# Kernel tuning notes

Hardware: AMD Instinct MI355X
Metric: run time of the kernel (lower is better)

Reference implementation:

```python
import jax, jax.numpy as jnp
import numpy as np

# Scalar-only irreps: 8x0e nodes in, 4x0e edge in, 8x0e edge out, 16x0e node out.
N = 50000          # nodes
E = 800000         # edges
MUL_NODE_IN = 8
MUL_EDGE_IN = 4
MUL_Z = 2 * MUL_NODE_IN          # cat([x[i], x[j]]) -> 16
MUL_EDGE_OUT = 8
MUL_NODE_OUT = 16
W_NUMEL = MUL_EDGE_IN * MUL_Z * MUL_EDGE_OUT  # 512 = edge_tp.weight_numel
RAD_IN, RAD_HID = 16, 64         # radial_neurons=[16, 64]


def setup_inputs() -> dict:
    key = jax.random.key(0)
    ks = jax.random.split(key, 7)
    x = jax.random.normal(ks[0], (N, MUL_NODE_IN), dtype=jnp.float32)
    edge_index = jax.random.randint(ks[1], (2, E), 0, N)
    edge_attr = jax.random.normal(ks[2], (E, MUL_EDGE_IN), dtype=jnp.float32)
    edge_len_emb = jax.random.normal(ks[3], (E, RAD_IN), dtype=jnp.float32)
    # radial MLP (e3nn FullyConnectedNet: normalized linear layers, silu)
    w1 = jax.random.normal(ks[4], (RAD_IN, RAD_HID), dtype=jnp.float32)
    w2 = jax.random.normal(ks[5], (RAD_HID, W_NUMEL), dtype=jnp.float32)
    # node_tp internal shared weights: [mul_node_in, mul_edge_out, mul_node_out]
    w_node = jax.random.normal(ks[6], (MUL_NODE_IN, MUL_EDGE_OUT, MUL_NODE_OUT), dtype=jnp.float32)
    return {"x": x, "edge_index": edge_index, "edge_attr": edge_attr,
            "edge_len_emb": edge_len_emb, "w1": w1, "w2": w2, "w_node": w_node}


def reference(x, edge_index, edge_attr, edge_len_emb, w1, w2, w_node):
    i, j = edge_index[0], edge_index[1]
    # radial MLP -> per-edge TP weights (e3nn normalized linears, silu)
    h = jax.nn.silu(edge_len_emb @ w1 / jnp.sqrt(jnp.float32(RAD_IN)))
    w_edge = (h @ w2 / jnp.sqrt(jnp.float32(RAD_HID)))
    w_edge = w_edge.reshape(E, MUL_EDGE_IN, MUL_Z, MUL_EDGE_OUT)
    # gather + concat: z = cat([x[i], x[j]])  [E, 16]
    z = jnp.concatenate([x[i], x[j]], axis=-1)
    # edge_tp: fully-connected scalar TP with path norm 1/sqrt(mul1*mul2)
    edge_out = jnp.einsum('ea,eb,eabk->ek', edge_attr, z, w_edge)
    edge_out = edge_out / jnp.sqrt(jnp.float32(MUL_EDGE_IN * MUL_Z))
    # scatter-sum to destination nodes j
    e_sum = jax.ops.segment_sum(edge_out, j, num_segments=x.shape[0])
    # node_tp: shared internal weights, path norm 1/sqrt(mul1*mul2)
    x_out = jnp.einsum('na,nb,abk->nk', x, e_sum, w_node)
    x_out = x_out / jnp.sqrt(jnp.float32(MUL_NODE_IN * MUL_EDGE_OUT))
    return (x_out, edge_out)
```

## Files before the change

kernel.cpp:

```cpp
#include <hip/hip_runtime.h>


typedef __attribute__((ext_vector_type(8))) short short8;
typedef __attribute__((ext_vector_type(4))) float floatx4;

__device__ inline unsigned short f2bf(float f) {
    union { float f; unsigned u; } v; v.f = f;
    unsigned r = v.u + 0x7FFFu + ((v.u >> 16) & 1u);
    return (unsigned short)(r >> 16);
}
__device__ inline float bf2f(unsigned short u) {
    union { unsigned u; float f; } v; v.u = ((unsigned)u) << 16;
    return v.f;
}

constexpr int TB   = 512;
constexpr int NBLK = 256;

constexpr int W2_LD = 72;
constexpr int HS_LD = 72;
constexpr int ZT_LD = 40;
constexpr int AT_LD = 40;

__global__ __launch_bounds__(TB, 2) void edge_kernel(
    const float* __restrict__ x,
    const int*   __restrict__ ei,
    const float* __restrict__ attr,
    const float* __restrict__ emb,
    const float* __restrict__ w1,
    const float* __restrict__ w2,
    float* __restrict__ edge_out,
    float* __restrict__ e_sum,
    int E)
{
    __shared__ __align__(16) unsigned short s_w2t[512 * W2_LD];
    __shared__ __align__(16) unsigned short s_hsA[8 * 32 * HS_LD];
    __shared__ __align__(16) unsigned short s_ztA[8 * 16 * ZT_LD];
    __shared__ __align__(16) unsigned short s_atA[8 * 4 * AT_LD];
    __shared__ __align__(16) int            s_vjA[8 * 32];

    const int tid  = threadIdx.x;
    const int wave = tid >> 6;
    const int lane = tid & 63;
    const int m16  = lane & 15;
    const int quad = lane >> 4;

    for (int idx = tid; idx < 512 * 64; idx += TB) {
        const int n = idx & 511, k = idx >> 9;
        s_w2t[n * W2_LD + k] = f2bf(w2[k * 512 + n]);
    }
    __syncthreads();

    short8 w1f[4];
    #pragma unroll
    for (int ct = 0; ct < 4; ++ct) {
        short8 f;
        if (quad < 2) {
            #pragma unroll
            for (int j = 0; j < 8; ++j)
                f[j] = (short)f2bf(w1[(quad * 8 + j) * 64 + ct * 16 + m16]);
        } else {
            #pragma unroll
            for (int j = 0; j < 8; ++j) f[j] = 0;
        }
        w1f[ct] = f;
    }

    unsigned short* hsw = s_hsA + wave * 32 * HS_LD;
    unsigned short* ztw = s_ztA + wave * 16 * ZT_LD;
    unsigned short* atw = s_atA + wave * 4 * AT_LD;
    int*            vjw = s_vjA + wave * 32;

    const int wid = blockIdx.x * 8 + wave;
    const int nw  = NBLK * 8;
    const int ntiles = E >> 5;

    for (int tile = wid; tile < ntiles; tile += nw) {
        const int base = tile << 5;

        if (quad < 2) {
            const int mst = quad * 16 + m16;
            const int e   = base + mst;
            const int vj  = ei[E + e];
            const float4 a4  = *(const float4*)(attr + (size_t)e * 4);
            const int vi  = ei[e];
            const float4 xi0 = *(const float4*)(x + (size_t)vi * 8);
            const float4 xi1 = *(const float4*)(x + (size_t)vi * 8 + 4);
            const float4 xj0 = *(const float4*)(x + (size_t)vj * 8);
            const float4 xj1 = *(const float4*)(x + (size_t)vj * 8 + 4);
            ztw[ 0*ZT_LD+mst]=f2bf(xi0.x); ztw[ 1*ZT_LD+mst]=f2bf(xi0.y);
            ztw[ 2*ZT_LD+mst]=f2bf(xi0.z); ztw[ 3*ZT_LD+mst]=f2bf(xi0.w);
            ztw[ 4*ZT_LD+mst]=f2bf(xi1.x); ztw[ 5*ZT_LD+mst]=f2bf(xi1.y);
            ztw[ 6*ZT_LD+mst]=f2bf(xi1.z); ztw[ 7*ZT_LD+mst]=f2bf(xi1.w);
            ztw[ 8*ZT_LD+mst]=f2bf(xj0.x); ztw[ 9*ZT_LD+mst]=f2bf(xj0.y);
            ztw[10*ZT_LD+mst]=f2bf(xj0.z); ztw[11*ZT_LD+mst]=f2bf(xj0.w);
            ztw[12*ZT_LD+mst]=f2bf(xj1.x); ztw[13*ZT_LD+mst]=f2bf(xj1.y);
            ztw[14*ZT_LD+mst]=f2bf(xj1.z); ztw[15*ZT_LD+mst]=f2bf(xj1.w);
            atw[0*AT_LD+mst]=f2bf(a4.x);   atw[1*AT_LD+mst]=f2bf(a4.y);
            atw[2*AT_LD+mst]=f2bf(a4.z);   atw[3*AT_LD+mst]=f2bf(a4.w);
            vjw[mst] = vj;
        }

        short8 a1[2];
        #pragma unroll
        for (int s = 0; s < 2; ++s) {
            short8 f;
            if (quad < 2) {
                const float* ep = emb + (size_t)(base + s * 16 + m16) * 16 + quad * 8;
                const float4 u0 = *(const float4*)ep;
                const float4 u1 = *(const float4*)(ep + 4);
                f[0]=(short)f2bf(u0.x); f[1]=(short)f2bf(u0.y);
                f[2]=(short)f2bf(u0.z); f[3]=(short)f2bf(u0.w);
                f[4]=(short)f2bf(u1.x); f[5]=(short)f2bf(u1.y);
                f[6]=(short)f2bf(u1.z); f[7]=(short)f2bf(u1.w);
            } else {
                #pragma unroll
                for (int j = 0; j < 8; ++j) f[j] = 0;
            }
            a1[s] = f;
        }

        #pragma unroll
        for (int s = 0; s < 2; ++s) {
            #pragma unroll
            for (int ct = 0; ct < 4; ++ct) {
                floatx4 c = {0.f, 0.f, 0.f, 0.f};
                c = __builtin_amdgcn_mfma_f32_16x16x32_bf16(a1[s], w1f[ct], c, 0, 0, 0);
                #pragma unroll
                for (int r = 0; r < 4; ++r) {
                    const float u  = c[r] * 0.25f;
                    const float sv = u / (1.f + __expf(-u)) * (1.0f / 64.0f);
                    hsw[(s * 16 + quad * 4 + r) * HS_LD + ct * 16 + m16] = f2bf(sv);
                }
            }
        }

        short8 a2[2][2];
        #pragma unroll
        for (int s = 0; s < 2; ++s)
            #pragma unroll
            for (int q = 0; q < 2; ++q)
                a2[s][q] = *(const short8*)(hsw + (s * 16 + m16) * HS_LD + q * 32 + quad * 8);

        float eacc[2][4];
        #pragma unroll
        for (int s = 0; s < 2; ++s)
            #pragma unroll
            for (int r = 0; r < 4; ++r) eacc[s][r] = 0.f;

        #pragma unroll 1
        for (int g = 0; g < 4; ++g) {
            float av[2][4];
            #pragma unroll
            for (int s = 0; s < 2; ++s) {
                const ushort4 a4v = *(const ushort4*)(atw + g * AT_LD + s * 16 + quad * 4);
                av[s][0] = bf2f(a4v.x); av[s][1] = bf2f(a4v.y);
                av[s][2] = bf2f(a4v.z); av[s][3] = bf2f(a4v.w);
            }
            #pragma unroll
            for (int tt = 0; tt < 8; ++tt) {
                const int t = g * 8 + tt;
                short8 b2[2];
                b2[0] = *(const short8*)(s_w2t + (16 * t + m16) * W2_LD + quad * 8);
                b2[1] = *(const short8*)(s_w2t + (16 * t + m16) * W2_LD + 32 + quad * 8);
                const int b_idx = (2 * t + (m16 >> 3)) & 15;
                #pragma unroll
                for (int s = 0; s < 2; ++s) {
                    floatx4 c = {0.f, 0.f, 0.f, 0.f};
                    c = __builtin_amdgcn_mfma_f32_16x16x32_bf16(a2[s][0], b2[0], c, 0, 0, 0);
                    c = __builtin_amdgcn_mfma_f32_16x16x32_bf16(a2[s][1], b2[1], c, 0, 0, 0);
                    const ushort4 zv = *(const ushort4*)(ztw + b_idx * ZT_LD + s * 16 + quad * 4);
                    eacc[s][0] += c[0] * (av[s][0] * bf2f(zv.x));
                    eacc[s][1] += c[1] * (av[s][1] * bf2f(zv.y));
                    eacc[s][2] += c[2] * (av[s][2] * bf2f(zv.z));
                    eacc[s][3] += c[3] * (av[s][3] * bf2f(zv.w));
                }
            }
        }

        #pragma unroll
        for (int s = 0; s < 2; ++s)
            #pragma unroll
            for (int r = 0; r < 4; ++r)
                eacc[s][r] += __shfl_xor(eacc[s][r], 8, 64);

        if (m16 < 8) {
            #pragma unroll
            for (int s = 0; s < 2; ++s) {
                const int4 vjq = *(const int4*)(vjw + s * 16 + quad * 4);
                const int vjr[4] = {vjq.x, vjq.y, vjq.z, vjq.w};
                #pragma unroll
                for (int r = 0; r < 4; ++r) {
                    const int e = base + s * 16 + quad * 4 + r;
                    edge_out[(size_t)e * 8 + m16] = eacc[s][r];
                    atomicAdd(e_sum + (size_t)vjr[r] * 8 + m16, eacc[s][r]);
                }
            }
        }
    }
}

__global__ __launch_bounds__(256) void node_kernel(
    const float* __restrict__ x,
    const float* __restrict__ e_sum,
    const float* __restrict__ w_node,
    float* __restrict__ x_out,
    int N)
{
    __shared__ float s_w[8 * 8 * 16];
    for (int idx = threadIdx.x; idx < 1024; idx += 256) s_w[idx] = w_node[idx];
    __syncthreads();

    const int n = blockIdx.x * 256 + threadIdx.x;
    if (n >= N) return;

    float xa[8], eb[8];
    #pragma unroll
    for (int a = 0; a < 8; ++a) xa[a] = x[(size_t)n * 8 + a];
    #pragma unroll
    for (int b = 0; b < 8; ++b) eb[b] = e_sum[(size_t)n * 8 + b];

    float out[16];
    #pragma unroll
    for (int k = 0; k < 16; ++k) out[k] = 0.f;

    const float4* wv = (const float4*)s_w;
    #pragma unroll
    for (int a = 0; a < 8; ++a) {
        #pragma unroll
        for (int b = 0; b < 8; ++b) {
            const float t = xa[a] * eb[b] * 0.125f;
            #pragma unroll
            for (int k4 = 0; k4 < 4; ++k4) {
                const float4 w = wv[(a * 8 + b) * 4 + k4];
                out[k4 * 4 + 0] = fmaf(t, w.x, out[k4 * 4 + 0]);
                out[k4 * 4 + 1] = fmaf(t, w.y, out[k4 * 4 + 1]);
                out[k4 * 4 + 2] = fmaf(t, w.z, out[k4 * 4 + 2]);
                out[k4 * 4 + 3] = fmaf(t, w.w, out[k4 * 4 + 3]);
            }
        }
    }

    float4* xo = (float4*)(x_out + (size_t)n * 16);
    #pragma unroll
    for (int k4 = 0; k4 < 4; ++k4)
        xo[k4] = make_float4(out[k4 * 4 + 0], out[k4 * 4 + 1],
                             out[k4 * 4 + 2], out[k4 * 4 + 3]);
}

extern "C" void kernel_launch(void* const* d_in, const int* in_sizes, int n_in,
                              void* d_out, int out_size, void* d_ws, size_t ws_size,
                              hipStream_t stream) {
    const float* x      = (const float*)d_in[0];
    const int*   ei     = (const int*)d_in[1];
    const float* attr   = (const float*)d_in[2];
    const float* emb    = (const float*)d_in[3];
    const float* w1     = (const float*)d_in[4];
    const float* w2     = (const float*)d_in[5];
    const float* w_node = (const float*)d_in[6];

    const int N = in_sizes[0] / 8;
    const int E = in_sizes[2] / 4;

    float* x_out    = (float*)d_out;
    float* edge_out = (float*)d_out + (size_t)N * 16;
    float* e_sum    = (float*)d_ws;

    hipMemsetAsync(e_sum, 0, (size_t)N * 8 * sizeof(float), stream);

    edge_kernel<<<NBLK, TB, 0, stream>>>(x, ei, attr, emb, w1, w2,
                                         edge_out, e_sum, E);

    node_kernel<<<(N + 255) / 256, 256, 0, stream>>>(x, e_sum, w_node, x_out, N);
}
```

Measured before the change: 221.2 us.

## Software-pipeline edge gathers across tiles and keep z/attr staging in fp32

Prefetches the next tile's node features, attributes and embeddings into registers, and the index pair for the tile after that, so gather latency overlaps the current tile's MFMA work. Staging for z and edge_attr moves from bf16 to fp32 shared memory, and the attr multiply is factored out of the inner loop via a per-group accumulator. It also uses packed bf16 conversion instructions, a reciprocal instead of a divide in the SiLU, and s_setprio around the MFMA loop. In exchange it raises register pressure and shared-memory footprint.

```diff
diff --git a/kernel.cpp b/kernel.cpp
--- a/kernel.cpp
+++ b/kernel.cpp
@@ -9,18 +9,20 @@
     unsigned r = v.u + 0x7FFFu + ((v.u >> 16) & 1u);
     return (unsigned short)(r >> 16);
 }
-__device__ inline float bf2f(unsigned short u) {
-    union { unsigned u; float f; } v; v.u = ((unsigned)u) << 16;
-    return v.f;
+
+__device__ inline unsigned cvt_pk_bf16(float lo, float hi) {
+    unsigned r;
+    asm("v_cvt_pk_bf16_f32 %0, %1, %2" : "=v"(r) : "v"(lo), "v"(hi));
+    return r;
 }
 
 constexpr int TB   = 512;
 constexpr int NBLK = 256;
 
-constexpr int W2_LD = 72;
-constexpr int HS_LD = 72;
-constexpr int ZT_LD = 40;
-constexpr int AT_LD = 40;
+constexpr int W2_LD  = 72;
+constexpr int HS_LD  = 72;
+constexpr int ZT_LDF = 48;
+constexpr int AT_LDF = 32;
 
 __global__ __launch_bounds__(TB, 2) void edge_kernel(
     const float* __restrict__ x,
@@ -35,15 +37,16 @@
 {
     __shared__ __align__(16) unsigned short s_w2t[512 * W2_LD];
     __shared__ __align__(16) unsigned short s_hsA[8 * 32 * HS_LD];
-    __shared__ __align__(16) unsigned short s_ztA[8 * 16 * ZT_LD];
-    __shared__ __align__(16) unsigned short s_atA[8 * 4 * AT_LD];
-    __shared__ __align__(16) int            s_vjA[8 * 32];
+    __shared__ __align__(16) float          s_ztA[8 * 16 * ZT_LDF];
+    __shared__ __align__(16) float          s_atA[8 * 4 * AT_LDF];
+    __shared__ int                          s_vjA[8 * 32];
 
     const int tid  = threadIdx.x;
     const int wave = tid >> 6;
     const int lane = tid & 63;
     const int m16  = lane & 15;
     const int quad = lane >> 4;
+    const int par  = m16 >> 3;
 
     for (int idx = tid; idx < 512 * 64; idx += TB) {
         const int n = idx & 511, k = idx >> 9;
@@ -67,57 +70,104 @@
     }
 
     unsigned short* hsw = s_hsA + wave * 32 * HS_LD;
-    unsigned short* ztw = s_ztA + wave * 16 * ZT_LD;
-    unsigned short* atw = s_atA + wave * 4 * AT_LD;
+    float*          ztw = s_ztA + wave * 16 * ZT_LDF;
+    float*          atw = s_atA + wave * 4 * AT_LDF;
     int*            vjw = s_vjA + wave * 32;
 
-    const int wid = blockIdx.x * 8 + wave;
-    const int nw  = NBLK * 8;
-    const int ntiles = E >> 5;
+    const int  wid = blockIdx.x * 8 + wave;
+    const int  nw  = NBLK * 8;
+    const int  ntiles = E >> 5;
+    const bool stg = (quad < 2);
+    const int  mst = quad * 16 + m16;
+
+    float4 xi0, xi1, xj0, xj1, a4;
+    float4 em0a, em0b, em1a, em1b;
+    int viN = 0, vjN = 0, vjC = 0;
+
+    if (wid < ntiles && stg) {
+        const int e0 = (wid << 5) + mst;
+        const int vi = ei[e0];
+        vjC = ei[E + e0];
+        xi0 = *(const float4*)(x + (size_t)vi * 8);
+        xi1 = *(const float4*)(x + (size_t)vi * 8 + 4);
+        xj0 = *(const float4*)(x + (size_t)vjC * 8);
+        xj1 = *(const float4*)(x + (size_t)vjC * 8 + 4);
+        a4  = *(const float4*)(attr + (size_t)e0 * 4);
+        const float* ep0 = emb + (size_t)((wid << 5) + m16) * 16 + quad * 8;
+        em0a = *(const float4*)ep0;
+        em0b = *(const float4*)(ep0 + 4);
+        const float* ep1 = emb + (size_t)((wid << 5) + 16 + m16) * 16 + quad * 8;
+        em1a = *(const float4*)ep1;
+        em1b = *(const float4*)(ep1 + 4);
+        const int t1 = (wid + nw < ntiles) ? (wid + nw) : wid;
+        const int e1 = (t1 << 5) + mst;
+        viN = ei[e1];
+        vjN = ei[E + e1];
+    }
 
     for (int tile = wid; tile < ntiles; tile += nw) {
         const int base = tile << 5;
 
-        if (quad < 2) {
-            const int mst = quad * 16 + m16;
-            const int e   = base + mst;
-            const int vj  = ei[E + e];
-            const float4 a4  = *(const float4*)(attr + (size_t)e * 4);
-            const int vi  = ei[e];
-            const float4 xi0 = *(const float4*)(x + (size_t)vi * 8);
-            const float4 xi1 = *(const float4*)(x + (size_t)vi * 8 + 4);
-            const float4 xj0 = *(const float4*)(x + (size_t)vj * 8);
-            const float4 xj1 = *(const float4*)(x + (size_t)vj * 8 + 4);
-            ztw[ 0*ZT_LD+mst]=f2bf(xi0.x); ztw[ 1*ZT_LD+mst]=f2bf(xi0.y);
-            ztw[ 2*ZT_LD+mst]=f2bf(xi0.z); ztw[ 3*ZT_LD+mst]=f2bf(xi0.w);
-            ztw[ 4*ZT_LD+mst]=f2bf(xi1.x); ztw[ 5*ZT_LD+mst]=f2bf(xi1.y);
-            ztw[ 6*ZT_LD+mst]=f2bf(xi1.z); ztw[ 7*ZT_LD+mst]=f2bf(xi1.w);
-            ztw[ 8*ZT_LD+mst]=f2bf(xj0.x); ztw[ 9*ZT_LD+mst]=f2bf(xj0.y);
-            ztw[10*ZT_LD+mst]=f2bf(xj0.z); ztw[11*ZT_LD+mst]=f2bf(xj0.w);
-            ztw[12*ZT_LD+mst]=f2bf(xj1.x); ztw[13*ZT_LD+mst]=f2bf(xj1.y);
-            ztw[14*ZT_LD+mst]=f2bf(xj1.z); ztw[15*ZT_LD+mst]=f2bf(xj1.w);
-            atw[0*AT_LD+mst]=f2bf(a4.x);   atw[1*AT_LD+mst]=f2bf(a4.y);
-            atw[2*AT_LD+mst]=f2bf(a4.z);   atw[3*AT_LD+mst]=f2bf(a4.w);
-            vjw[mst] = vj;
+        if (stg) {
+            ztw[ 0*ZT_LDF+mst]=xi0.x; ztw[ 1*ZT_LDF+mst]=xi0.y;
+            ztw[ 2*ZT_LDF+mst]=xi0.z; ztw[ 3*ZT_LDF+mst]=xi0.w;
+            ztw[ 4*ZT_LDF+mst]=xi1.x; ztw[ 5*ZT_LDF+mst]=xi1.y;
+            ztw[ 6*ZT_LDF+mst]=xi1.z; ztw[ 7*ZT_LDF+mst]=xi1.w;
+            ztw[ 8*ZT_LDF+mst]=xj0.x; ztw[ 9*ZT_LDF+mst]=xj0.y;
+            ztw[10*ZT_LDF+mst]=xj0.z; ztw[11*ZT_LDF+mst]=xj0.w;
+            ztw[12*ZT_LDF+mst]=xj1.x; ztw[13*ZT_LDF+mst]=xj1.y;
+            ztw[14*ZT_LDF+mst]=xj1.z; ztw[15*ZT_LDF+mst]=xj1.w;
+            atw[0*AT_LDF+mst]=a4.x;   atw[1*AT_LDF+mst]=a4.y;
+            atw[2*AT_LDF+mst]=a4.z;   atw[3*AT_LDF+mst]=a4.w;
+            vjw[mst] = vjC;
         }
 
         short8 a1[2];
-        #pragma unroll
-        for (int s = 0; s < 2; ++s) {
-            short8 f;
-            if (quad < 2) {
-                const float* ep = emb + (size_t)(base + s * 16 + m16) * 16 + quad * 8;
-                const float4 u0 = *(const float4*)ep;
-                const float4 u1 = *(const float4*)(ep + 4);
-                f[0]=(short)f2bf(u0.x); f[1]=(short)f2bf(u0.y);
-                f[2]=(short)f2bf(u0.z); f[3]=(short)f2bf(u0.w);
-                f[4]=(short)f2bf(u1.x); f[5]=(short)f2bf(u1.y);
-                f[6]=(short)f2bf(u1.z); f[7]=(short)f2bf(u1.w);
+        {
+            union { short8 s8; unsigned u[4]; } uu;
+            if (stg) {
+                uu.u[0] = cvt_pk_bf16(em0a.x, em0a.y);
+                uu.u[1] = cvt_pk_bf16(em0a.z, em0a.w);
+                uu.u[2] = cvt_pk_bf16(em0b.x, em0b.y);
+                uu.u[3] = cvt_pk_bf16(em0b.z, em0b.w);
             } else {
-                #pragma unroll
-                for (int j = 0; j < 8; ++j) f[j] = 0;
-            }
-            a1[s] = f;
+                uu.u[0]=0u; uu.u[1]=0u; uu.u[2]=0u; uu.u[3]=0u;
+            }
+            a1[0] = uu.s8;
+            if (stg) {
+                uu.u[0] = cvt_pk_bf16(em1a.x, em1a.y);
+                uu.u[1] = cvt_pk_bf16(em1a.z, em1a.w);
+                uu.u[2] = cvt_pk_bf16(em1b.x, em1b.y);
+                uu.u[3] = cvt_pk_bf16(em1b.z, em1b.w);
+            } else {
+                uu.u[0]=0u; uu.u[1]=0u; uu.u[2]=0u; uu.u[3]=0u;
+            }
+            a1[1] = uu.s8;
+        }
+
+        {
+            const int tn     = tile + nw;
+            const int tn_cl  = (tn  < ntiles) ? tn  : tile;
+            const int tnn    = tn + nw;
+            const int tnn_cl = (tnn < ntiles) ? tnn : tn_cl;
+            if (stg) {
+                const int en = (tn_cl << 5) + mst;
+                vjC = vjN;
+                xi0 = *(const float4*)(x + (size_t)viN * 8);
+                xi1 = *(const float4*)(x + (size_t)viN * 8 + 4);
+                xj0 = *(const float4*)(x + (size_t)vjN * 8);
+                xj1 = *(const float4*)(x + (size_t)vjN * 8 + 4);
+                a4  = *(const float4*)(attr + (size_t)en * 4);
+                const float* ep0 = emb + (size_t)((tn_cl << 5) + m16) * 16 + quad * 8;
+                em0a = *(const float4*)ep0;
+                em0b = *(const float4*)(ep0 + 4);
+                const float* ep1 = emb + (size_t)((tn_cl << 5) + 16 + m16) * 16 + quad * 8;
+                em1a = *(const float4*)ep1;
+                em1b = *(const float4*)(ep1 + 4);
+                const int enn = (tnn_cl << 5) + mst;
+                viN = ei[enn];
+                vjN = ei[E + enn];
+            }
         }
 
         #pragma unroll
@@ -126,12 +176,21 @@
             for (int ct = 0; ct < 4; ++ct) {
                 floatx4 c = {0.f, 0.f, 0.f, 0.f};
                 c = __builtin_amdgcn_mfma_f32_16x16x32_bf16(a1[s], w1f[ct], c, 0, 0, 0);
+                float sv[4];
                 #pragma unroll
                 for (int r = 0; r < 4; ++r) {
-                    const float u  = c[r] * 0.25f;
-                    const float sv = u / (1.f + __expf(-u)) * (1.0f / 64.0f);
-                    hsw[(s * 16 + quad * 4 + r) * HS_LD + ct * 16 + m16] = f2bf(sv);
+                    const float u   = c[r] * 0.25f;
+                    const float den = 1.f + __expf(-u);
+                    sv[r] = u * __builtin_amdgcn_rcpf(den) * 0.015625f;
                 }
+                const unsigned p01 = cvt_pk_bf16(sv[0], sv[1]);
+                const unsigned p23 = cvt_pk_bf16(sv[2], sv[3]);
+                const int col  = ct * 16 + m16;
+                const int row0 = s * 16 + quad * 4;
+                hsw[(row0 + 0) * HS_LD + col] = (unsigned short)p01;
+                hsw[(row0 + 1) * HS_LD + col] = (unsigned short)(p01 >> 16);
+                hsw[(row0 + 2) * HS_LD + col] = (unsigned short)p23;
+                hsw[(row0 + 3) * HS_LD + col] = (unsigned short)(p23 >> 16);
             }
         }
 
@@ -148,35 +207,48 @@
             #pragma unroll
             for (int r = 0; r < 4; ++r) eacc[s][r] = 0.f;
 
+        __builtin_amdgcn_s_setprio(1);
         #pragma unroll 1
         for (int g = 0; g < 4; ++g) {
             float av[2][4];
             #pragma unroll
             for (int s = 0; s < 2; ++s) {
-                const ushort4 a4v = *(const ushort4*)(atw + g * AT_LD + s * 16 + quad * 4);
-                av[s][0] = bf2f(a4v.x); av[s][1] = bf2f(a4v.y);
-                av[s][2] = bf2f(a4v.z); av[s][3] = bf2f(a4v.w);
-            }
+                const float4 a4v = *(const float4*)(atw + g * AT_LDF + s * 16 + quad * 4);
+                av[s][0] = a4v.x; av[s][1] = a4v.y;
+                av[s][2] = a4v.z; av[s][3] = a4v.w;
+            }
+            float tacc[2][4];
+            #pragma unroll
+            for (int s = 0; s < 2; ++s)
+                #pragma unroll
+                for (int r = 0; r < 4; ++r) tacc[s][r] = 0.f;
+
             #pragma unroll
             for (int tt = 0; tt < 8; ++tt) {
                 const int t = g * 8 + tt;
                 short8 b2[2];
                 b2[0] = *(const short8*)(s_w2t + (16 * t + m16) * W2_LD + quad * 8);
                 b2[1] = *(const short8*)(s_w2t + (16 * t + m16) * W2_LD + 32 + quad * 8);
-                const int b_idx = (2 * t + (m16 >> 3)) & 15;
+                const int b_idx = (2 * tt + par) & 15;
                 #pragma unroll
                 for (int s = 0; s < 2; ++s) {
                     floatx4 c = {0.f, 0.f, 0.f, 0.f};
                     c = __builtin_amdgcn_mfma_f32_16x16x32_bf16(a2[s][0], b2[0], c, 0, 0, 0);
                     c = __builtin_amdgcn_mfma_f32_16x16x32_bf16(a2[s][1], b2[1], c, 0, 0, 0);
-                    const ushort4 zv = *(const ushort4*)(ztw + b_idx * ZT_LD + s * 16 + quad * 4);
-                    eacc[s][0] += c[0] * (av[s][0] * bf2f(zv.x));
-                    eacc[s][1] += c[1] * (av[s][1] * bf2f(zv.y));
-                    eacc[s][2] += c[2] * (av[s][2] * bf2f(zv.z));
-                    eacc[s][3] += c[3] * (av[s][3] * bf2f(zv.w));
+                    const float4 zv = *(const float4*)(ztw + b_idx * ZT_LDF + s * 16 + quad * 4);
+                    tacc[s][0] = fmaf(c[0], zv.x, tacc[s][0]);
+                    tacc[s][1] = fmaf(c[1], zv.y, tacc[s][1]);
+                    tacc[s][2] = fmaf(c[2], zv.z, tacc[s][2]);
+                    tacc[s][3] = fmaf(c[3], zv.w, tacc[s][3]);
                 }
             }
-        }
+            #pragma unroll
+            for (int s = 0; s < 2; ++s)
+                #pragma unroll
+                for (int r = 0; r < 4; ++r)
+                    eacc[s][r] = fmaf(av[s][r], tacc[s][r], eacc[s][r]);
+        }
+        __builtin_amdgcn_s_setprio(0);
 
         #pragma unroll
         for (int s = 0; s < 2; ++s)
```

After: 190.8 us. -13.8%, faster.
